# Kernel tuning notes

Hardware: AMD Instinct MI355X
Metric: run time of the kernel (lower is better)

## Reference

```python
import jax, jax.numpy as jnp
import numpy as np

NUM_HEADS = 8  # from init_kwargs


def setup_inputs() -> dict:
    key = jax.random.key(0)
    ks = jax.random.split(key, 8)
    B, N, Din, H, Dout, E = 4, 2048, 256, 512, 256, 65536
    s = 0.02
    return {
        "x": jax.random.normal(ks[0], (B, N, Din), jnp.float32),
        "edge_index": jax.random.randint(ks[1], (2, E), 0, N),
        "W_gcn": jax.random.normal(ks[2], (Din, H), jnp.float32) * s,
        "b_gcn": jnp.zeros((H,), jnp.float32),
        "in_proj_w": jax.random.normal(ks[3], (3 * H, H), jnp.float32) * s,
        "in_proj_b": jnp.zeros((3 * H,), jnp.float32),
        "out_proj_w": jax.random.normal(ks[4], (H, H), jnp.float32) * s,
        "out_proj_b": jnp.zeros((H,), jnp.float32),
        "fc_w": jax.random.normal(ks[5], (H, Dout), jnp.float32) * s,
        "fc_b": jnp.zeros((Dout,), jnp.float32),
    }


def _gcn(x, edge_index, W, b):
    # PyG GCNConv: add self-loops, symmetric normalization, gather-scatter aggregation.
    B, N, _ = x.shape
    loop = jnp.arange(N)
    src = jnp.concatenate([edge_index[0], loop])  # message source j
    dst = jnp.concatenate([edge_index[1], loop])  # aggregation target i
    deg = jnp.zeros((N,), x.dtype).at[dst].add(1.0)
    dinv = jnp.where(deg > 0, jax.lax.rsqrt(deg), 0.0)
    norm = dinv[src] * dinv[dst]                  # [Etot]
    xl = x @ W                                    # [B, N, H]
    msgs = xl[:, src, :] * norm[None, :, None]    # [B, Etot, H]
    out = jnp.zeros_like(xl).at[:, dst].add(msgs)  # scatter-add over edges
    return out + b


def _mha(x_nbh, wi, bi, wo, bo, nh):
    # torch MultiheadAttention, input [N(seq), B, H], self-attention.
    N, B, H = x_nbh.shape
    dh = H // nh
    qkv = x_nbh @ wi.T + bi                       # [N, B, 3H]
    q, k, v = jnp.split(qkv, 3, axis=-1)
    q = q.reshape(N, B, nh, dh) * (dh ** -0.5)
    k = k.reshape(N, B, nh, dh)
    v = v.reshape(N, B, nh, dh)
    scores = jnp.einsum("nbhd,mbhd->bhnm", q, k)  # [B, nh, N, N]
    attn = jax.nn.softmax(scores, axis=-1)
    o = jnp.einsum("bhnm,mbhd->nbhd", attn, v).reshape(N, B, H)
    return o @ wo.T + bo


def reference(x, edge_index, W_gcn, b_gcn, in_proj_w, in_proj_b,
              out_proj_w, out_proj_b, fc_w, fc_b):
    h = _gcn(x, edge_index, W_gcn, b_gcn)         # [B, N, H]
    h = jnp.transpose(h, (1, 0, 2))               # [N, B, H]
    h = _mha(h, in_proj_w, in_proj_b, out_proj_w, out_proj_b, NUM_HEADS)
    h = jnp.transpose(h, (1, 0, 2))               # [B, N, H]
    h = jax.nn.relu(h)
    return h @ fc_w + fc_b                        # [B, N, Dout]
```

## Files before the change

kernel.cpp:

```cpp
#include <hip/hip_runtime.h>
#include <hip/hip_bf16.h>


#define NN 2048
#define HH 512
#define NHEAD 8
#define DH 64

typedef _Float16 f16;
typedef __attribute__((ext_vector_type(2))) _Float16 f16x2;
typedef __attribute__((ext_vector_type(4))) _Float16 f16x4;
typedef __attribute__((ext_vector_type(8))) _Float16 f16x8;
typedef __attribute__((ext_vector_type(4))) float f32x4;

#define GLOAD_LDS16(g, l)                                              \
  __builtin_amdgcn_global_load_lds(                                    \
      (const __attribute__((address_space(1))) void*)(g),              \
      (__attribute__((address_space(3))) void*)(l), 16, 0, 0)

__device__ __forceinline__ float fast_exp2(float x) {
#if __has_builtin(__builtin_amdgcn_exp2f)
  return __builtin_amdgcn_exp2f(x);
#else
  return exp2f(x);
#endif
}

__device__ __forceinline__ f16x2 cvt_pk_f16(float a, float b) {
#if __has_builtin(__builtin_amdgcn_cvt_pkrtz)
  return __builtin_bit_cast(f16x2, __builtin_amdgcn_cvt_pkrtz(a, b));
#else
  f16x2 r = { (f16)a, (f16)b };
  return r;
#endif
}


__global__ __launch_bounds__(256) void prep_cvt_kernel(const float* __restrict__ wi,
                                                       const float* __restrict__ wo,
                                                       f16* __restrict__ wi16,
                                                       f16* __restrict__ wo16,
                                                       float* __restrict__ deg,
                                                       int* __restrict__ cursor) {
  const int bid = blockIdx.x, t = threadIdx.x;
  if (bid < 768) {
    const int i = bid * 256 + t;
    const float4 v = ((const float4*)wi)[i];
    f16x4 o = { (f16)v.x, (f16)v.y, (f16)v.z, (f16)v.w };
    ((f16x4*)wi16)[i] = o;
  } else if (bid < 1024) {
    const int i = (bid - 768) * 256 + t;
    const float4 v = ((const float4*)wo)[i];
    f16x4 o = { (f16)v.x, (f16)v.y, (f16)v.z, (f16)v.w };
    ((f16x4*)wo16)[i] = o;
  } else {
    for (int i = t; i < NN; i += 256) { deg[i] = 1.0f; cursor[i] = 0; }
  }
}

__global__ __launch_bounds__(256) void prep_transpose_kernel(const float* __restrict__ wg,
                                                             const float* __restrict__ fcw,
                                                             f16* __restrict__ wg16t,
                                                             f16* __restrict__ fcw16t) {
  __shared__ float tbuf[32][33];
  const float* in;
  f16* outp;
  int R, C, bx, by;
  if (blockIdx.x < 128) { in = wg;  outp = wg16t;  R = 256; C = 512;
                          bx = blockIdx.x & 15; by = blockIdx.x >> 4; }
  else { int id = blockIdx.x - 128; in = fcw; outp = fcw16t; R = 512; C = 256;
         bx = id & 7; by = id >> 3; }
  const int c0 = bx * 32, r0 = by * 32;
  const int tx = threadIdx.x & 31, ty = threadIdx.x >> 5;
#pragma unroll
  for (int i = 0; i < 32; i += 8) tbuf[ty + i][tx] = in[(size_t)(r0 + ty + i) * C + c0 + tx];
  __syncthreads();
#pragma unroll
  for (int i = 0; i < 32; i += 8)
    outp[(size_t)(c0 + ty + i) * R + r0 + tx] = (f16)tbuf[tx][ty + i];
}


__global__ __launch_bounds__(256) void count_deg_kernel(const int* __restrict__ ei, int E,
                                                        float* __restrict__ deg) {
  int e = blockIdx.x * 256 + threadIdx.x;
  if (e < E) atomicAdd(&deg[ei[E + e]], 1.0f);
}

__global__ __launch_bounds__(1024) void build_rowptr_kernel(const float* __restrict__ deg,
                                                            float* __restrict__ dinv,
                                                            int* __restrict__ rowptr) {
  __shared__ int a[NN];
  __shared__ int bbuf[NN];
  const int t = threadIdx.x;
  for (int i = t; i < NN; i += 1024) {
    float dg = deg[i];
    a[i] = (int)dg - 1;
    dinv[i] = rsqrtf(dg);
  }
  __syncthreads();
  int* src = a;
  int* dst = bbuf;
  for (int off = 1; off < NN; off <<= 1) {
    for (int i = t; i < NN; i += 1024) {
      int v = src[i];
      if (i >= off) v += src[i - off];
      dst[i] = v;
    }
    __syncthreads();
    int* tmp = src; src = dst; dst = tmp;
  }
  for (int i = t; i < NN; i += 1024) rowptr[i + 1] = src[i];
  if (t == 0) rowptr[0] = 0;
}

__global__ __launch_bounds__(256) void fill_csr_kernel(const int* __restrict__ ei, int E,
                                                       const int* __restrict__ rowptr,
                                                       int* __restrict__ cursor,
                                                       int* __restrict__ csr_src) {
  int e = blockIdx.x * 256 + threadIdx.x;
  if (e < E) {
    int s = ei[e];
    int d = ei[E + e];
    int pos = atomicAdd(&cursor[d], 1);
    csr_src[rowptr[d] + pos] = s;
  }
}


template <int OUTMODE, bool BIAS, bool RELU, bool AF32, int MT = 128>
__global__ __launch_bounds__(256) void mfma_gemm_kernel(
    const void* __restrict__ Ap, const f16* __restrict__ Bt,
    const float* __restrict__ bias, void* __restrict__ Cout,
    int M, int N, int K,
    f16* __restrict__ q_out, f16* __restrict__ k_out, f16* __restrict__ v_out) {
  constexpr int MI = MT / 32;
  __shared__ f16 As[MT * 32];
  __shared__ f16 Bs[128 * 32];
  const int tid = threadIdx.x;
  const int wave = tid >> 6, lane = tid & 63;
  const int quad = lane >> 4, l16 = lane & 15;
  const int m0 = blockIdx.y * MT, n0 = blockIdx.x * 128;
  const int moff = (wave >> 1) * (MI * 16), noff = (wave & 1) * 64;

  f32x4 acc[MI][4];
#pragma unroll
  for (int i = 0; i < MI; ++i)
#pragma unroll
    for (int j = 0; j < 4; ++j) acc[i][j] = (f32x4){0.f, 0.f, 0.f, 0.f};

  const int rpw = MT / 4;
  const int srowA = rpw * wave + (lane >> 2);
  const int srowB = 32 * wave + (lane >> 2);
  const int kch = (lane & 3) * 8;
  const f16* Ag = (const f16*)Ap + (size_t)(m0 + srowA) * K + kch;
  const float* Ag32 = (const float*)Ap + (size_t)(m0 + srowA) * K + kch;
  const f16* Bg = Bt + (size_t)(n0 + srowB) * K + kch;
  f16* As_w = &As[(rpw * wave) * 32];
  f16* Bs_w = &Bs[(32 * wave) * 32];

  for (int k0 = 0; k0 < K; k0 += 32) {
    __syncthreads();
    if (AF32) {
#pragma unroll
      for (int t = 0; t < 2; ++t) {
        const float* g = Ag32 + k0 + (size_t)(16 * t) * K;
        const float4 u0 = *(const float4*)g;
        const float4 u1 = *(const float4*)(g + 4);
        f16x8 o = { (f16)u0.x, (f16)u0.y, (f16)u0.z, (f16)u0.w,
                    (f16)u1.x, (f16)u1.y, (f16)u1.z, (f16)u1.w };
        *(f16x8*)&As[(srowA + 16 * t) * 32 + kch] = o;
      }
    } else {
      GLOAD_LDS16(Ag + k0, As_w);
      if (MT == 128) GLOAD_LDS16(Ag + k0 + (size_t)16 * K, As_w + 16 * 32);
    }
    GLOAD_LDS16(Bg + k0, Bs_w);
    GLOAD_LDS16(Bg + k0 + (size_t)16 * K, Bs_w + 16 * 32);
    __syncthreads();
    f16x8 af[MI], bf[4];
#pragma unroll
    for (int m16 = 0; m16 < MI; ++m16)
      af[m16] = *(const f16x8*)&As[(moff + m16 * 16 + l16) * 32 + quad * 8];
#pragma unroll
    for (int n16 = 0; n16 < 4; ++n16)
      bf[n16] = *(const f16x8*)&Bs[(noff + n16 * 16 + l16) * 32 + quad * 8];
#pragma unroll
    for (int m16 = 0; m16 < MI; ++m16)
#pragma unroll
      for (int n16 = 0; n16 < 4; ++n16)
        acc[m16][n16] =
            __builtin_amdgcn_mfma_f32_16x16x32_f16(af[m16], bf[n16], acc[m16][n16], 0, 0, 0);
  }

  float bv[4];
#pragma unroll
  for (int n16 = 0; n16 < 4; ++n16)
    bv[n16] = BIAS ? bias[n0 + noff + n16 * 16 + l16] : 0.f;

  if (OUTMODE == 2) {
    const int hblk = (n0 >> 6) + (wave & 1);
    const int which = hblk >> 3, h = hblk & 7;
    f16* dst = (which == 0) ? q_out : (which == 1) ? k_out : v_out;
    const float scale = (which == 0) ? 0.125f * 1.44269504088896340736f : 1.0f;
#pragma unroll
    for (int m16 = 0; m16 < MI; ++m16) {
#pragma unroll
      for (int r = 0; r < 4; ++r) {
        const int m = m0 + moff + m16 * 16 + quad * 4 + r;
        const int b = m >> 11, ns = m & 2047;
        f16* row = dst + ((size_t)(b * 8 + h) * NN + ns) * DH;
#pragma unroll
        for (int n16 = 0; n16 < 4; ++n16) {
          const int d = n16 * 16 + l16;
          row[d] = (f16)((acc[m16][n16][r] + bv[n16]) * scale);
        }
      }
    }
  } else {
#pragma unroll
    for (int m16 = 0; m16 < MI; ++m16) {
#pragma unroll
      for (int r = 0; r < 4; ++r) {
        const size_t row = (size_t)(m0 + moff + m16 * 16 + quad * 4 + r) * N;
#pragma unroll
        for (int n16 = 0; n16 < 4; ++n16) {
          const int col = n0 + noff + n16 * 16 + l16;
          float v = acc[m16][n16][r] + bv[n16];
          if (RELU) v = fmaxf(v, 0.f);
          if (OUTMODE == 0) ((float*)Cout)[row + col] = v;
          else ((f16*)Cout)[row + col] = (f16)v;
        }
      }
    }
  }
}


__global__ __launch_bounds__(256) void gcn_aggregate_kernel(const f16* __restrict__ xl,
                                                            const float* __restrict__ dinv,
                                                            const int* __restrict__ rowptr,
                                                            const int* __restrict__ csr_src,
                                                            const float* __restrict__ b_gcn,
                                                            f16* __restrict__ out) {
  __shared__ int s_src[256];
  __shared__ float s_dv[256];
  const int i = blockIdx.x;
  const int tid = threadIdx.x;
  const float dv_i = dinv[i];
  const int f = tid * 2;
  float ax[4], ay[4];
#pragma unroll
  for (int b = 0; b < 4; ++b) {
    const f16x2 self = *(const f16x2*)&xl[((size_t)(b * NN) + i) * HH + f];
    ax[b] = (float)self.x * dv_i;
    ay[b] = (float)self.y * dv_i;
  }
  const int beg = rowptr[i], end = rowptr[i + 1];
  for (int c0 = beg; c0 < end; c0 += 256) {
    const int cnt = min(256, end - c0);
    __syncthreads();
    if (tid < cnt) {
      int s = csr_src[c0 + tid];
      s_src[tid] = s;
      s_dv[tid] = dinv[s];
    }
    __syncthreads();
    for (int t = 0; t < cnt; ++t) {
      const int row = s_src[t];
      const float w = s_dv[t];
#pragma unroll
      for (int b = 0; b < 4; ++b) {
        const f16x2 v = *(const f16x2*)&xl[((size_t)(b * NN) + row) * HH + f];
        ax[b] = fmaf((float)v.x, w, ax[b]);
        ay[b] = fmaf((float)v.y, w, ay[b]);
      }
    }
  }
  const float2 bg = *(const float2*)&b_gcn[f];
#pragma unroll
  for (int b = 0; b < 4; ++b) {
    f16x2 o = { (f16)(ax[b] * dv_i + bg.x), (f16)(ay[b] * dv_i + bg.y) };
    *(f16x2*)&out[((size_t)(b * NN) + i) * HH + f] = o;
  }
}


__global__ __launch_bounds__(512) void flash_attn_f16_kernel(const f16* __restrict__ Qb,
                                                             const f16* __restrict__ Kb,
                                                             const f16* __restrict__ Vb,
                                                             f16* __restrict__ out) {
  const int LDK = 72;
  const int LDV = 136;
  __shared__ f16 Ks[128 * LDK];
  __shared__ f16 Vt[64 * LDV];
  const int tid = threadIdx.x;
  const int wave = tid >> 6, lane = tid & 63;
  const int quad = lane >> 4, l16 = lane & 15;
  const int bid = blockIdx.x;
  const int sw = (bid & 7) * 64 + (bid >> 3);
  const int bh = sw >> 4;
  const int n0 = (sw & 15) * 128;
  const int b = bh >> 3, h = bh & 7;
  const f16* kb = Kb + (size_t)bh * NN * DH;
  const f16* vb = Vb + (size_t)bh * NN * DH;

  f16x8 aq0, aq1;
  {
    const f16* qf = Qb + ((size_t)bh * NN + n0 + wave * 16 + l16) * DH + quad * 8;
    aq0 = *(const f16x8*)qf;
    aq1 = *(const f16x8*)(qf + 32);
  }

  float l_part = 0.f;
  f32x4 acc_o[4];
#pragma unroll
  for (int n16 = 0; n16 < 4; ++n16) acc_o[n16] = (f32x4){0.f, 0.f, 0.f, 0.f};

  const int krow = tid >> 3, kcol = (tid & 7) * 8;
  const int vdg = tid & 15, jb = tid >> 4;
  const int sb4 = (jb >> 3) * 32 + (jb & 3) * 8 + ((jb >> 2) & 1) * 4;

  f16x8 kreg0, kreg1;
  f16x4 vreg[4];
  {
    kreg0 = *(const f16x8*)(kb + (size_t)krow * DH + kcol);
    kreg1 = *(const f16x8*)(kb + (size_t)(64 + krow) * DH + kcol);
#pragma unroll
    for (int i = 0; i < 4; ++i)
      vreg[i] = *(const f16x4*)(vb + (size_t)(jb * 4 + i) * DH + vdg * 4);
  }

  for (int kt = 0; kt < NN / 128; ++kt) {
    __syncthreads();
    *(f16x8*)&Ks[krow * LDK + kcol] = kreg0;
    *(f16x8*)&Ks[(64 + krow) * LDK + kcol] = kreg1;
#pragma unroll
    for (int c = 0; c < 4; ++c) {
      f16x4 o = { vreg[0][c], vreg[1][c], vreg[2][c], vreg[3][c] };
      *(f16x4*)&Vt[(vdg * 4 + c) * LDV + sb4] = o;
    }
    if (kt + 1 < NN / 128) {
      const int k0n = (kt + 1) * 128;
      kreg0 = *(const f16x8*)(kb + (size_t)(k0n + krow) * DH + kcol);
      kreg1 = *(const f16x8*)(kb + (size_t)(k0n + 64 + krow) * DH + kcol);
#pragma unroll
      for (int i = 0; i < 4; ++i)
        vreg[i] = *(const f16x4*)(vb + (size_t)(k0n + jb * 4 + i) * DH + vdg * 4);
    }
    __syncthreads();
#pragma unroll
    for (int p = 0; p < 4; ++p) {
      f32x4 sA[2];
#pragma unroll
      for (int t = 0; t < 2; ++t) {
        const f16x8 ak0 = *(const f16x8*)&Ks[(p * 32 + t * 16 + l16) * LDK + quad * 8];
        const f16x8 ak1 = *(const f16x8*)&Ks[(p * 32 + t * 16 + l16) * LDK + quad * 8 + 32];
        f32x4 s = {0.f, 0.f, 0.f, 0.f};
        s = __builtin_amdgcn_mfma_f32_16x16x32_f16(ak0, aq0, s, 0, 0, 0);
        s = __builtin_amdgcn_mfma_f32_16x16x32_f16(ak1, aq1, s, 0, 0, 0);
        sA[t] = s;
      }
      f16x8 bvv[4];
#pragma unroll
      for (int n16 = 0; n16 < 4; ++n16)
        bvv[n16] = *(const f16x8*)&Vt[(n16 * 16 + l16) * LDV + p * 32 + quad * 8];
      union { f16x8 v; f16x2 h[4]; } ap;
      float sum = 0.f;
#pragma unroll
      for (int t = 0; t < 2; ++t)
#pragma unroll
        for (int rr = 0; rr < 2; ++rr) {
          const float e0 = fast_exp2(sA[t][rr * 2]);
          const float e1 = fast_exp2(sA[t][rr * 2 + 1]);
          sum += e0 + e1;
          ap.h[t * 2 + rr] = cvt_pk_f16(e0, e1);
        }
      l_part += sum;
#pragma unroll
      for (int n16 = 0; n16 < 4; ++n16)
        acc_o[n16] = __builtin_amdgcn_mfma_f32_16x16x32_f16(ap.v, bvv[n16], acc_o[n16], 0, 0, 0);
    }
  }
  float lp = l_part;
  lp += __shfl_xor(lp, 16);
  lp += __shfl_xor(lp, 32);
  f16* obase = out + ((size_t)b * NN + n0 + wave * 16) * HH + h * DH;
#pragma unroll
  for (int r = 0; r < 4; ++r) {
    const float lr = __shfl(lp, (lane & 48) | (quad * 4 + r));
    const float inv = 1.0f / lr;
#pragma unroll
    for (int n16 = 0; n16 < 4; ++n16)
      obase[(size_t)(quad * 4 + r) * HH + n16 * 16 + l16] = (f16)(acc_o[n16][r] * inv);
  }
}


extern "C" void kernel_launch(void* const* d_in, const int* in_sizes, int n_in,
                              void* d_out, int out_size, void* d_ws, size_t ws_size,
                              hipStream_t stream) {
  const float* x     = (const float*)d_in[0];
  const int*   ei    = (const int*)d_in[1];
  const float* W_gcn = (const float*)d_in[2];
  const float* b_gcn = (const float*)d_in[3];
  const float* wi    = (const float*)d_in[4];
  const float* bi    = (const float*)d_in[5];
  const float* wo    = (const float*)d_in[6];
  const float* bo    = (const float*)d_in[7];
  const float* fcw   = (const float*)d_in[8];
  const float* fcb   = (const float*)d_in[9];
  float* out = (float*)d_out;
  const int E = in_sizes[1] / 2;
  const int M = 4 * NN;

  char* wsb = (char*)d_ws;
  const size_t MB = 1u << 20;
  f16* xl16   = (f16*)(wsb + 4 * MB);
  f16* hb16   = (f16*)(wsb + 12 * MB);
  f16* Qb     = (f16*)(wsb + 20 * MB);
  f16* Kb     = (f16*)(wsb + 28 * MB);
  f16* Vb     = (f16*)(wsb + 36 * MB);
  f16* attn16 = (f16*)(wsb + 44 * MB);
  f16* proj16 = (f16*)(wsb + 52 * MB);
  f16* wi16   = (f16*)(wsb + 60 * MB);
  f16* wo16   = (f16*)(wsb + 62 * MB);
  f16* wg16t  = (f16*)(wsb + 63 * MB);
  f16* fcw16t = (f16*)(wsb + 64 * MB);
  float* deg  = (float*)(wsb + 65 * MB);
  float* dinv = deg + NN;
  int* rowptr = (int*)(dinv + NN);
  int* cursor = rowptr + 2080;
  int* csr    = cursor + NN;

  prep_cvt_kernel<<<1025, 256, 0, stream>>>(wi, wo, wi16, wo16, deg, cursor);
  prep_transpose_kernel<<<256, 256, 0, stream>>>(W_gcn, fcw, wg16t, fcw16t);

  count_deg_kernel<<<(E + 255) / 256, 256, 0, stream>>>(ei, E, deg);
  build_rowptr_kernel<<<1, 1024, 0, stream>>>(deg, dinv, rowptr);
  fill_csr_kernel<<<(E + 255) / 256, 256, 0, stream>>>(ei, E, rowptr, cursor, csr);

  mfma_gemm_kernel<1, false, false, true><<<dim3(4, 64), 256, 0, stream>>>(
      x, wg16t, nullptr, xl16, M, 512, 256, nullptr, nullptr, nullptr);
  gcn_aggregate_kernel<<<NN, 256, 0, stream>>>(xl16, dinv, rowptr, csr, b_gcn, hb16);
  mfma_gemm_kernel<2, true, false, false><<<dim3(12, 64), 256, 0, stream>>>(
      hb16, wi16, bi, nullptr, M, 1536, 512, Qb, Kb, Vb);
  flash_attn_f16_kernel<<<512, 512, 0, stream>>>(Qb, Kb, Vb, attn16);
  mfma_gemm_kernel<1, true, true, false><<<dim3(4, 64), 256, 0, stream>>>(
      attn16, wo16, bo, proj16, M, 512, 512, nullptr, nullptr, nullptr);
  mfma_gemm_kernel<0, true, false, false, 64><<<dim3(2, 128), 256, 0, stream>>>(
      proj16, fcw16t, fcb, out, M, 256, 512, nullptr, nullptr, nullptr);
}
```

Measured before the change: 258.0 us.

## Double-buffer LDS in flash attention and vectorize GCN aggregation loads

The attention kernel now keeps two LDS buffers for K and V. The next tile's global loads are issued before compute, and the stores into the alternate buffer happen mid-iteration, which drops one barrier per tile so memory latency overlaps MFMA work. The GCN aggregation kernel is remapped so each thread handles one batch and 8 contiguous features with 16-byte loads, instead of 2 features across all 4 batches with 4-byte loads. The cost is double the attention LDS (about 35KB) and different gather access patterns in the GCN kernel.

```diff
diff --git a/kernel.cpp b/kernel.cpp
--- a/kernel.cpp
+++ b/kernel.cpp
@@ -248,13 +248,14 @@
   const int i = blockIdx.x;
   const int tid = threadIdx.x;
   const float dv_i = dinv[i];
-  const int f = tid * 2;
-  float ax[4], ay[4];
-#pragma unroll
-  for (int b = 0; b < 4; ++b) {
-    const f16x2 self = *(const f16x2*)&xl[((size_t)(b * NN) + i) * HH + f];
-    ax[b] = (float)self.x * dv_i;
-    ay[b] = (float)self.y * dv_i;
+  const int b = tid >> 6;
+  const int f = (tid & 63) * 8;
+  const f16* xb = xl + (size_t)(b * NN) * HH + f;
+  float acc[8];
+  {
+    const f16x8 self = *(const f16x8*)&xb[(size_t)i * HH];
+#pragma unroll
+    for (int j = 0; j < 8; ++j) acc[j] = (float)self[j] * dv_i;
   }
   const int beg = rowptr[i], end = rowptr[i + 1];
   for (int c0 = beg; c0 < end; c0 += 256) {
@@ -267,22 +268,24 @@
     }
     __syncthreads();
     for (int t = 0; t < cnt; ++t) {
-      const int row = s_src[t];
+      const f16x8 v = *(const f16x8*)&xb[(size_t)s_src[t] * HH];
       const float w = s_dv[t];
 #pragma unroll
-      for (int b = 0; b < 4; ++b) {
-        const f16x2 v = *(const f16x2*)&xl[((size_t)(b * NN) + row) * HH + f];
-        ax[b] = fmaf((float)v.x, w, ax[b]);
-        ay[b] = fmaf((float)v.y, w, ay[b]);
-      }
-    }
-  }
-  const float2 bg = *(const float2*)&b_gcn[f];
-#pragma unroll
-  for (int b = 0; b < 4; ++b) {
-    f16x2 o = { (f16)(ax[b] * dv_i + bg.x), (f16)(ay[b] * dv_i + bg.y) };
-    *(f16x2*)&out[((size_t)(b * NN) + i) * HH + f] = o;
-  }
+      for (int j = 0; j < 8; ++j) acc[j] = fmaf((float)v[j], w, acc[j]);
+    }
+  }
+  const float4 bg0 = *(const float4*)&b_gcn[f];
+  const float4 bg1 = *(const float4*)&b_gcn[f + 4];
+  f16x8 o;
+  o[0] = (f16)(acc[0] * dv_i + bg0.x);
+  o[1] = (f16)(acc[1] * dv_i + bg0.y);
+  o[2] = (f16)(acc[2] * dv_i + bg0.z);
+  o[3] = (f16)(acc[3] * dv_i + bg0.w);
+  o[4] = (f16)(acc[4] * dv_i + bg1.x);
+  o[5] = (f16)(acc[5] * dv_i + bg1.y);
+  o[6] = (f16)(acc[6] * dv_i + bg1.z);
+  o[7] = (f16)(acc[7] * dv_i + bg1.w);
+  *(f16x8*)&out[((size_t)(b * NN) + i) * HH + f] = o;
 }
 
 
@@ -290,10 +293,10 @@
                                                              const f16* __restrict__ Kb,
                                                              const f16* __restrict__ Vb,
                                                              f16* __restrict__ out) {
-  const int LDK = 72;
-  const int LDV = 136;
-  __shared__ f16 Ks[128 * LDK];
-  __shared__ f16 Vt[64 * LDV];
+  constexpr int LDK = 72;
+  constexpr int LDV = 136;
+  __shared__ f16 Ks[2][128 * LDK];
+  __shared__ f16 Vt[2][64 * LDV];
   const int tid = threadIdx.x;
   const int wave = tid >> 6, lane = tid & 63;
   const int quad = lane >> 4, l16 = lane & 15;
@@ -323,65 +326,72 @@
 
   f16x8 kreg0, kreg1;
   f16x4 vreg[4];
-  {
-    kreg0 = *(const f16x8*)(kb + (size_t)krow * DH + kcol);
-    kreg1 = *(const f16x8*)(kb + (size_t)(64 + krow) * DH + kcol);
+
+  auto load_tile = [&](int k0) {
+    kreg0 = *(const f16x8*)(kb + (size_t)(k0 + krow) * DH + kcol);
+    kreg1 = *(const f16x8*)(kb + (size_t)(k0 + 64 + krow) * DH + kcol);
 #pragma unroll
     for (int i = 0; i < 4; ++i)
-      vreg[i] = *(const f16x4*)(vb + (size_t)(jb * 4 + i) * DH + vdg * 4);
-  }
-
-  for (int kt = 0; kt < NN / 128; ++kt) {
-    __syncthreads();
-    *(f16x8*)&Ks[krow * LDK + kcol] = kreg0;
-    *(f16x8*)&Ks[(64 + krow) * LDK + kcol] = kreg1;
+      vreg[i] = *(const f16x4*)(vb + (size_t)(k0 + jb * 4 + i) * DH + vdg * 4);
+  };
+  auto store_tile = [&](int buf) {
+    *(f16x8*)&Ks[buf][krow * LDK + kcol] = kreg0;
+    *(f16x8*)&Ks[buf][(64 + krow) * LDK + kcol] = kreg1;
 #pragma unroll
     for (int c = 0; c < 4; ++c) {
       f16x4 o = { vreg[0][c], vreg[1][c], vreg[2][c], vreg[3][c] };
-      *(f16x4*)&Vt[(vdg * 4 + c) * LDV + sb4] = o;
-    }
-    if (kt + 1 < NN / 128) {
-      const int k0n = (kt + 1) * 128;
-      kreg0 = *(const f16x8*)(kb + (size_t)(k0n + krow) * DH + kcol);
-      kreg1 = *(const f16x8*)(kb + (size_t)(k0n + 64 + krow) * DH + kcol);
-#pragma unroll
-      for (int i = 0; i < 4; ++i)
-        vreg[i] = *(const f16x4*)(vb + (size_t)(k0n + jb * 4 + i) * DH + vdg * 4);
-    }
-    __syncthreads();
-#pragma unroll
-    for (int p = 0; p < 4; ++p) {
-      f32x4 sA[2];
-#pragma unroll
-      for (int t = 0; t < 2; ++t) {
-        const f16x8 ak0 = *(const f16x8*)&Ks[(p * 32 + t * 16 + l16) * LDK + quad * 8];
-        const f16x8 ak1 = *(const f16x8*)&Ks[(p * 32 + t * 16 + l16) * LDK + quad * 8 + 32];
-        f32x4 s = {0.f, 0.f, 0.f, 0.f};
-        s = __builtin_amdgcn_mfma_f32_16x16x32_f16(ak0, aq0, s, 0, 0, 0);
-        s = __builtin_amdgcn_mfma_f32_16x16x32_f16(ak1, aq1, s, 0, 0, 0);
-        sA[t] = s;
+      *(f16x4*)&Vt[buf][(vdg * 4 + c) * LDV + sb4] = o;
+    }
+  };
+  auto do_p = [&](int p, int cur) {
+    const f16* KsC = &Ks[cur][0];
+    const f16* VtC = &Vt[cur][0];
+    f32x4 sA[2];
+#pragma unroll
+    for (int t = 0; t < 2; ++t) {
+      const f16x8 ak0 = *(const f16x8*)&KsC[(p * 32 + t * 16 + l16) * LDK + quad * 8];
+      const f16x8 ak1 = *(const f16x8*)&KsC[(p * 32 + t * 16 + l16) * LDK + quad * 8 + 32];
+      f32x4 s = {0.f, 0.f, 0.f, 0.f};
+      s = __builtin_amdgcn_mfma_f32_16x16x32_f16(ak0, aq0, s, 0, 0, 0);
+      s = __builtin_amdgcn_mfma_f32_16x16x32_f16(ak1, aq1, s, 0, 0, 0);
+      sA[t] = s;
+    }
+    f16x8 bvv[4];
+#pragma unroll
+    for (int n16 = 0; n16 < 4; ++n16)
+      bvv[n16] = *(const f16x8*)&VtC[(n16 * 16 + l16) * LDV + p * 32 + quad * 8];
+    union { f16x8 v; f16x2 hh[4]; } ap;
+    float sum = 0.f;
+#pragma unroll
+    for (int t = 0; t < 2; ++t)
+#pragma unroll
+      for (int rr = 0; rr < 2; ++rr) {
+        const float e0 = fast_exp2(sA[t][rr * 2]);
+        const float e1 = fast_exp2(sA[t][rr * 2 + 1]);
+        sum += e0 + e1;
+        ap.hh[t * 2 + rr] = cvt_pk_f16(e0, e1);
       }
-      f16x8 bvv[4];
-#pragma unroll
-      for (int n16 = 0; n16 < 4; ++n16)
-        bvv[n16] = *(const f16x8*)&Vt[(n16 * 16 + l16) * LDV + p * 32 + quad * 8];
-      union { f16x8 v; f16x2 h[4]; } ap;
-      float sum = 0.f;
-#pragma unroll
-      for (int t = 0; t < 2; ++t)
-#pragma unroll
-        for (int rr = 0; rr < 2; ++rr) {
-          const float e0 = fast_exp2(sA[t][rr * 2]);
-          const float e1 = fast_exp2(sA[t][rr * 2 + 1]);
-          sum += e0 + e1;
-          ap.h[t * 2 + rr] = cvt_pk_f16(e0, e1);
-        }
-      l_part += sum;
-#pragma unroll
-      for (int n16 = 0; n16 < 4; ++n16)
-        acc_o[n16] = __builtin_amdgcn_mfma_f32_16x16x32_f16(ap.v, bvv[n16], acc_o[n16], 0, 0, 0);
-    }
-  }
+    l_part += sum;
+#pragma unroll
+    for (int n16 = 0; n16 < 4; ++n16)
+      acc_o[n16] = __builtin_amdgcn_mfma_f32_16x16x32_f16(ap.v, bvv[n16], acc_o[n16], 0, 0, 0);
+  };
+
+  load_tile(0);
+  store_tile(0);
+  int cur = 0;
+  for (int kt = 0; kt < NN / 128; ++kt) {
+    __syncthreads();
+    const bool pf = (kt + 1) < (NN / 128);
+    if (pf) load_tile((kt + 1) * 128);
+    do_p(0, cur);
+    do_p(1, cur);
+    if (pf) store_tile(cur ^ 1);
+    do_p(2, cur);
+    do_p(3, cur);
+    cur ^= 1;
+  }
+
   float lp = l_part;
   lp += __shfl_xor(lp, 16);
   lp += __shfl_xor(lp, 32);
```

New measurement: 247.8 us. 1.04x faster.
